# Optimization experiments

Hardware: AMD Instinct MI355X
Metric: run time of the kernel (lower is better)

Reference implementation:

```python
import jax, jax.numpy as jnp
import numpy as np

D = 1024      # d_model
H = 16        # n_heads
HD = D // H   # head_dim = 64
B = 2
NQ = 2048     # prod(spatial_shape_q)
NK = 2048     # prod(spatial_shape_kv)
SCALE_BASE_Q = 2 * NQ   # spatial_shape_q[0] * 2
SCALE_BASE_K = 2 * NK   # spatial_shape_kv[0] * 2
THETA = 10000.0         # theta_rescale_factor=1.0 -> theta unchanged


def _init_freqs(dim):
    # learned_freq=True: parameter initialized to standard rotary frequencies
    return 1.0 / (THETA ** (jnp.arange(0, dim, 2, dtype=jnp.float32) / dim))


def _rotate_half(x):
    # interleaved pair rotation: (x1, x2) -> (-x2, x1)
    x1 = x[..., ::2]
    x2 = x[..., 1::2]
    return jnp.stack((-x2, x1), axis=-1).reshape(x.shape)


def _apply_rope_xpos(x, freqs_param, scale_base, sign):
    # x: (B, H, N, HD); freqs_param: (HD//2,)
    n = x.shape[2]
    dim = x.shape[-1]
    t = jnp.arange(n, dtype=jnp.float32)
    freqs = jnp.repeat(t[:, None] * freqs_param[None, :], 2, axis=-1)  # (N, HD)
    # xpos length-extrapolatable scaling
    power = (t - n // 2) / scale_base                                   # (N,)
    sv = (jnp.arange(0, dim, 2, dtype=jnp.float32) + 0.4 * dim) / (1.4 * dim)
    scale = jnp.repeat(sv[None, :] ** power[:, None], 2, axis=-1) ** sign  # (N, HD)
    return x * jnp.cos(freqs) * scale + _rotate_half(x) * jnp.sin(freqs) * scale


def setup_inputs() -> dict:
    key = jax.random.key(0)
    ks = jax.random.split(key, 10)
    s = 0.02
    return {
        "q_seq": jax.random.normal(ks[0], (B, NQ, D), jnp.float32),
        "kv_seq": jax.random.normal(ks[1], (B, NK, D), jnp.float32),
        "Wq": jax.random.normal(ks[2], (D, D), jnp.float32) * s,
        "bq": jnp.zeros((D,), jnp.float32),
        "Wk": jax.random.normal(ks[3], (D, D), jnp.float32) * s,
        "bk": jnp.zeros((D,), jnp.float32),
        "Wv": jax.random.normal(ks[4], (D, D), jnp.float32) * s,
        "bv": jnp.zeros((D,), jnp.float32),
        "Wo": jax.random.normal(ks[5], (D, D), jnp.float32) * s,
        "bo": jnp.zeros((D,), jnp.float32),
        "freqs_q": _init_freqs(HD),
        "freqs_kv": _init_freqs(HD),
    }


def reference(q_seq, kv_seq, Wq, bq, Wk, bk, Wv, bv, Wo, bo, freqs_q, freqs_kv):
    Bq, Nq, C = q_seq.shape
    Nk = kv_seq.shape[1]
    q = (q_seq @ Wq.T + bq).reshape(Bq, Nq, H, HD).transpose(0, 2, 1, 3)
    k = (kv_seq @ Wk.T + bk).reshape(Bq, Nk, H, HD).transpose(0, 2, 1, 3)
    v = (kv_seq @ Wv.T + bv).reshape(Bq, Nk, H, HD).transpose(0, 2, 1, 3)
    q = _apply_rope_xpos(q, freqs_q, SCALE_BASE_Q, sign=1.0)   # queries: scale^{+1}
    k = _apply_rope_xpos(k, freqs_kv, SCALE_BASE_K, sign=-1.0)  # keys: scale^{-1}
    attn = jax.nn.softmax(
        jnp.einsum("bhqd,bhkd->bhqk", q, k) * (HD ** -0.5), axis=-1
    )
    out = jnp.einsum("bhqk,bhkd->bhqd", attn, v)
    out = out.transpose(0, 2, 1, 3).reshape(Bq, Nq, C)
    return (out @ Wo.T + bo, attn)
```

## Files before the change

kernel.cpp:

```cpp
#include <hip/hip_runtime.h>

#define NQ 2048
#define NKK 2048
#define DD 1024
#define HH 16

typedef __attribute__((ext_vector_type(8))) short bf16x8;
typedef __attribute__((ext_vector_type(4))) float f32x4;

__device__ __forceinline__ short f2bf(float f){
    union { float f; unsigned u; } v; v.f = f;
    unsigned u = v.u + 0x7FFFu + ((v.u >> 16) & 1u);
    return (short)(u >> 16);
}
__device__ __forceinline__ float bf2f(unsigned short u){
    union { unsigned u; float f; } v; v.u = ((unsigned)u) << 16;
    return v.f;
}

__global__ __launch_bounds__(256) void cvt_bf16(const float* __restrict__ src,
                                                short* __restrict__ dst, int n){
    int i = (blockIdx.x * 256 + threadIdx.x) * 4;
    if (i < n){
        float4 v = *(const float4*)(src + i);
        union { short s[4]; uint2 u; } o;
        o.s[0] = f2bf(v.x); o.s[1] = f2bf(v.y);
        o.s[2] = f2bf(v.z); o.s[3] = f2bf(v.w);
        *(uint2*)(dst + i) = o.u;
    }
}

__global__ __launch_bounds__(256) void rope_kernel(const short* __restrict__ x,
                                                   short* __restrict__ y,
                                                   const float* __restrict__ fr,
                                                   int N, float scale_base,
                                                   float sign, float prescale){
    int p = blockIdx.x * 256 + threadIdx.x;
    int col2 = p & 511;
    int row  = p >> 9;
    int n    = row & (N - 1);
    int i    = col2 & 31;
    float t  = (float)n;
    float fv = t * fr[i];
    float c = cosf(fv), s = sinf(fv);
    float power = (t - (float)(N / 2)) / scale_base;
    float sv = ((float)(2 * i) + 0.4f * 64.f) / (1.4f * 64.f);
    float scale = exp2f(sign * power * log2f(sv)) * prescale;
    unsigned xv = *(const unsigned*)(x + 2 * (size_t)p);
    float x0 = bf2f((unsigned short)(xv & 0xFFFFu));
    float x1 = bf2f((unsigned short)(xv >> 16));
    float y0 = (x0 * c - x1 * s) * scale;
    float y1 = (x1 * c + x0 * s) * scale;
    unsigned o = (unsigned)(unsigned short)f2bf(y0) |
                 ((unsigned)(unsigned short)f2bf(y1) << 16);
    *(unsigned*)(y + 2 * (size_t)p) = o;
}

template<bool F32OUT>
__global__ __launch_bounds__(256) void gemm_bt(const short* __restrict__ A,
                                               const short* __restrict__ W,
                                               const float* __restrict__ bias,
                                               void* __restrict__ Cout,
                                               int M, int N, int K){
    __shared__ __align__(16) short lA[128 * 72];
    __shared__ __align__(16) short lB[128 * 72];
    int tid = threadIdx.x;
    int wave = tid >> 6, lane = tid & 63;
    int l16 = lane & 15, quad = lane >> 4;
    int wr = wave >> 1, wc = wave & 1;
    int row0 = blockIdx.y * 128, col0 = blockIdx.x * 128;

    f32x4 acc[4][4];
#pragma unroll
    for (int a = 0; a < 4; a++)
#pragma unroll
        for (int b = 0; b < 4; b++) acc[a][b] = (f32x4){0.f, 0.f, 0.f, 0.f};

    for (int k0 = 0; k0 < K; k0 += 64){
#pragma unroll
        for (int r = 0; r < 4; r++){
            int e = r * 2048 + tid * 8;
            int ar = e >> 6, ac = e & 63;
            *(uint4*)&lA[ar * 72 + ac] = *(const uint4*)(A + (size_t)(row0 + ar) * K + k0 + ac);
            *(uint4*)&lB[ar * 72 + ac] = *(const uint4*)(W + (size_t)(col0 + ar) * K + k0 + ac);
        }
        __syncthreads();
#pragma unroll
        for (int kk = 0; kk < 2; kk++){
            bf16x8 af[4], bfr[4];
#pragma unroll
            for (int t = 0; t < 4; t++){
                af[t]  = *(const bf16x8*)&lA[(wr * 64 + t * 16 + l16) * 72 + kk * 32 + quad * 8];
                bfr[t] = *(const bf16x8*)&lB[(wc * 64 + t * 16 + l16) * 72 + kk * 32 + quad * 8];
            }
#pragma unroll
            for (int tm = 0; tm < 4; tm++)
#pragma unroll
                for (int tn = 0; tn < 4; tn++)
                    acc[tm][tn] = __builtin_amdgcn_mfma_f32_16x16x32_bf16(af[tm], bfr[tn], acc[tm][tn], 0, 0, 0);
        }
        __syncthreads();
    }
#pragma unroll
    for (int tm = 0; tm < 4; tm++){
        int gr = row0 + wr * 64 + tm * 16 + quad * 4;
#pragma unroll
        for (int tn = 0; tn < 4; tn++){
            int gc = col0 + wc * 64 + tn * 16 + l16;
            float bv = bias[gc];
#pragma unroll
            for (int r = 0; r < 4; r++){
                float v = acc[tm][tn][r] + bv;
                if (F32OUT) ((float*)Cout)[(size_t)(gr + r) * N + gc] = v;
                else        ((short*)Cout)[(size_t)(gr + r) * N + gc] = f2bf(v);
            }
        }
    }
}

__global__ __launch_bounds__(256) void transpose_v(const short* __restrict__ vp,
                                                   short* __restrict__ vT){
    int kt = blockIdx.x;
    int bh = blockIdx.y;
    int b = bh >> 4, h = bh & 15;
    int tid = threadIdx.x;
    int hd = tid & 63;
#pragma unroll
    for (int it = 0; it < 16; it++){
        int kl = (tid >> 6) + it * 4;
        int k = kt * 64 + kl;
        short v = vp[((size_t)(b * NKK + k)) * DD + h * 64 + hd];
        vT[((size_t)(bh * 64 + hd)) * NKK + k] = v;
    }
}

__global__ __launch_bounds__(256) void attn_kernel(const short* __restrict__ qp,
                                                   const short* __restrict__ kp,
                                                   const short* __restrict__ vT,
                                                   float* __restrict__ attn,
                                                   short* __restrict__ op){
    __shared__ __align__(16) short lK[64 * 72];
    __shared__ __align__(16) short lV[64 * 72];
    __shared__ __align__(16) short lP[64 * 72];
    __shared__ float lMf[64], lLi[64];

    int qt = blockIdx.x;
    int bh = blockIdx.y;
    int b = bh >> 4, h = bh & 15;
    int tid = threadIdx.x, wave = tid >> 6, lane = tid & 63;
    int l16 = lane & 15, quad = lane >> 4;

    int q0 = qt * 64;
    int qrow = q0 + wave * 16 + l16;
    const short* qb = qp + ((size_t)(b * NQ + qrow)) * DD + h * 64;
    bf16x8 qf[2];
    qf[0] = *(const bf16x8*)(qb + quad * 8);
    qf[1] = *(const bf16x8*)(qb + 32 + quad * 8);

    const short* kb = kp + ((size_t)(b * NKK)) * DD + h * 64;
    const short* vb = vT + ((size_t)(bh * 64)) * NKK;

    float m = -1e30f, l = 0.f;
    for (int kt = 0; kt < 32; kt++){
#pragma unroll
        for (int rnd = 0; rnd < 2; rnd++){
            int e = rnd * 2048 + tid * 8;
            int kr = e >> 6, kc = e & 63;
            *(uint4*)&lK[kr * 72 + kc] = *(const uint4*)(kb + (size_t)(kt * 64 + kr) * DD + kc);
        }
        __syncthreads();
        f32x4 St[4];
#pragma unroll
        for (int t = 0; t < 4; t++){
            f32x4 a = (f32x4){0.f, 0.f, 0.f, 0.f};
#pragma unroll
            for (int kk = 0; kk < 2; kk++){
                bf16x8 kf = *(const bf16x8*)&lK[(t * 16 + l16) * 72 + kk * 32 + quad * 8];
                a = __builtin_amdgcn_mfma_f32_16x16x32_bf16(kf, qf[kk], a, 0, 0, 0);
            }
            St[t] = a;
        }
        float mx = m;
#pragma unroll
        for (int t = 0; t < 4; t++)
#pragma unroll
            for (int r = 0; r < 4; r++) mx = fmaxf(mx, St[t][r]);
        float sum = 0.f;
#pragma unroll
        for (int t = 0; t < 4; t++)
#pragma unroll
            for (int r = 0; r < 4; r++) sum += __expf(St[t][r] - mx);
        l = l * __expf(m - mx) + sum;
        m = mx;
        __syncthreads();
    }
    float M = fmaxf(m, __shfl_xor(m, 16, 64));
    M = fmaxf(M, __shfl_xor(M, 32, 64));
    float ls = l * __expf(m - M);
    ls += __shfl_xor(ls, 16, 64);
    ls += __shfl_xor(ls, 32, 64);
    if (quad == 0){ lMf[wave * 16 + l16] = M; lLi[wave * 16 + l16] = 1.f / ls; }
    __syncthreads();
    float mf[4], il[4];
#pragma unroll
    for (int r = 0; r < 4; r++){
        mf[r] = lMf[wave * 16 + quad * 4 + r];
        il[r] = lLi[wave * 16 + quad * 4 + r];
    }

    f32x4 O[4];
#pragma unroll
    for (int th = 0; th < 4; th++) O[th] = (f32x4){0.f, 0.f, 0.f, 0.f};
    float* ab = attn + (((size_t)bh * NQ) + q0 + wave * 16) * NKK;

    for (int kt = 0; kt < 32; kt++){
#pragma unroll
        for (int rnd = 0; rnd < 2; rnd++){
            int e = rnd * 2048 + tid * 8;
            int kr = e >> 6, kc = e & 63;
            *(uint4*)&lK[kr * 72 + kc] = *(const uint4*)(kb + (size_t)(kt * 64 + kr) * DD + kc);
            *(uint4*)&lV[kr * 72 + kc] = *(const uint4*)(vb + (size_t)kr * NKK + kt * 64 + kc);
        }
        __syncthreads();
        f32x4 S[4];
#pragma unroll
        for (int tn = 0; tn < 4; tn++){
            f32x4 a = (f32x4){0.f, 0.f, 0.f, 0.f};
#pragma unroll
            for (int kk = 0; kk < 2; kk++){
                bf16x8 kf = *(const bf16x8*)&lK[(tn * 16 + l16) * 72 + kk * 32 + quad * 8];
                a = __builtin_amdgcn_mfma_f32_16x16x32_bf16(qf[kk], kf, a, 0, 0, 0);
            }
            S[tn] = a;
        }
#pragma unroll
        for (int tn = 0; tn < 4; tn++){
#pragma unroll
            for (int r = 0; r < 4; r++){
                float p = __expf(S[tn][r] - mf[r]) * il[r];
                ab[(size_t)(quad * 4 + r) * NKK + kt * 64 + tn * 16 + l16] = p;
                lP[(wave * 16 + quad * 4 + r) * 72 + tn * 16 + l16] = f2bf(p);
            }
        }
#pragma unroll
        for (int kk = 0; kk < 2; kk++){
            bf16x8 pf = *(const bf16x8*)&lP[(wave * 16 + l16) * 72 + kk * 32 + quad * 8];
#pragma unroll
            for (int th = 0; th < 4; th++){
                bf16x8 vf = *(const bf16x8*)&lV[(th * 16 + l16) * 72 + kk * 32 + quad * 8];
                O[th] = __builtin_amdgcn_mfma_f32_16x16x32_bf16(pf, vf, O[th], 0, 0, 0);
            }
        }
        __syncthreads();
    }
#pragma unroll
    for (int th = 0; th < 4; th++){
#pragma unroll
        for (int r = 0; r < 4; r++){
            int q = q0 + wave * 16 + quad * 4 + r;
            op[((size_t)(b * NQ + q)) * DD + h * 64 + th * 16 + l16] = f2bf(O[th][r]);
        }
    }
}

extern "C" void kernel_launch(void* const* d_in, const int* in_sizes, int n_in,
                              void* d_out, int out_size, void* d_ws, size_t ws_size,
                              hipStream_t stream) {
    const float* q_seq = (const float*)d_in[0];
    const float* kv_seq = (const float*)d_in[1];
    const float* Wq = (const float*)d_in[2];
    const float* bq = (const float*)d_in[3];
    const float* Wk = (const float*)d_in[4];
    const float* bk = (const float*)d_in[5];
    const float* Wv = (const float*)d_in[6];
    const float* bv = (const float*)d_in[7];
    const float* Wo = (const float*)d_in[8];
    const float* bo = (const float*)d_in[9];
    const float* freqs_q = (const float*)d_in[10];
    const float* freqs_kv = (const float*)d_in[11];

    float* out0 = (float*)d_out;
    float* attn = (float*)d_out + 4194304;

    short* qb  = (short*)d_ws;
    short* kvb = qb  + 4194304;
    short* wqb = kvb + 4194304;
    short* wkb = wqb + 1048576;
    short* wvb = wkb + 1048576;
    short* wob = wvb + 1048576;
    short* tmp = wob + 1048576;
    short* qpb = tmp + 4194304;
    short* kpb = qpb + 4194304;
    short* vpb = kpb + 4194304;
    short* vTb = qb;
    short* opb = tmp;

    cvt_bf16<<<4096, 256, 0, stream>>>(q_seq, qb, 4194304);
    cvt_bf16<<<4096, 256, 0, stream>>>(kv_seq, kvb, 4194304);
    cvt_bf16<<<1024, 256, 0, stream>>>(Wq, wqb, 1048576);
    cvt_bf16<<<1024, 256, 0, stream>>>(Wk, wkb, 1048576);
    cvt_bf16<<<1024, 256, 0, stream>>>(Wv, wvb, 1048576);
    cvt_bf16<<<1024, 256, 0, stream>>>(Wo, wob, 1048576);

    dim3 ggrid(8, 32);
    gemm_bt<false><<<ggrid, 256, 0, stream>>>(qb, wqb, bq, tmp, 4096, 1024, 1024);
    rope_kernel<<<8192, 256, 0, stream>>>(tmp, qpb, freqs_q, NQ, 4096.f, 1.f, 0.125f);
    gemm_bt<false><<<ggrid, 256, 0, stream>>>(kvb, wkb, bk, tmp, 4096, 1024, 1024);
    rope_kernel<<<8192, 256, 0, stream>>>(tmp, kpb, freqs_kv, NKK, 4096.f, -1.f, 1.f);
    gemm_bt<false><<<ggrid, 256, 0, stream>>>(kvb, wvb, bv, vpb, 4096, 1024, 1024);
    transpose_v<<<dim3(32, 32), 256, 0, stream>>>(vpb, vTb);
    attn_kernel<<<dim3(32, 32), 256, 0, stream>>>(qpb, kpb, vTb, attn, opb);
    gemm_bt<true><<<ggrid, 256, 0, stream>>>(opb, wob, bo, out0, 4096, 1024, 1024);
}
```

Measured before the change: 887.8 us.

## Use direct global-to-LDS loads, double-buffer GEMM, tile V transpose, vectorize attn stores

The GEMM switches to global_load_lds direct loads into double-buffered unpadded LDS tiles, so the next K tile is prefetched while the current one is computed. The V transpose now goes through an LDS tile, giving coalesced 16-byte reads and writes. The attention kernel loads K/V with direct-to-LDS loads and stages the fp32 probabilities in LDS, so the attn matrix is written with vectorized nontemporal 16-byte stores instead of scattered scalar stores. Removing the LDS padding may add bank conflicts on fragment reads, and the larger fp32 staging buffer raises LDS use.

```diff
diff --git a/kernel.cpp b/kernel.cpp
--- a/kernel.cpp
+++ b/kernel.cpp
@@ -16,6 +16,13 @@
 __device__ __forceinline__ float bf2f(unsigned short u){
     union { unsigned u; float f; } v; v.u = ((unsigned)u) << 16;
     return v.f;
+}
+
+__device__ __forceinline__ void gload16(const void* g, void* l){
+    __builtin_amdgcn_global_load_lds(
+        (__attribute__((address_space(1))) void*)g,
+        (__attribute__((address_space(3))) void*)l,
+        16, 0, 0);
 }
 
 __global__ __launch_bounds__(256) void cvt_bf16(const float* __restrict__ src,
@@ -62,36 +69,48 @@
                                                const float* __restrict__ bias,
                                                void* __restrict__ Cout,
                                                int M, int N, int K){
-    __shared__ __align__(16) short lA[128 * 72];
-    __shared__ __align__(16) short lB[128 * 72];
+    __shared__ __align__(16) short lA[2][128 * 64];
+    __shared__ __align__(16) short lB[2][128 * 64];
     int tid = threadIdx.x;
     int wave = tid >> 6, lane = tid & 63;
     int l16 = lane & 15, quad = lane >> 4;
     int wr = wave >> 1, wc = wave & 1;
     int row0 = blockIdx.y * 128, col0 = blockIdx.x * 128;
 
+    const short* Ab = A + (size_t)(row0 + wave * 32 + (lane >> 3)) * K + (lane & 7) * 8;
+    const short* Wb = W + (size_t)(col0 + wave * 32 + (lane >> 3)) * K + (lane & 7) * 8;
+
     f32x4 acc[4][4];
 #pragma unroll
     for (int a = 0; a < 4; a++)
 #pragma unroll
         for (int b = 0; b < 4; b++) acc[a][b] = (f32x4){0.f, 0.f, 0.f, 0.f};
 
-    for (int k0 = 0; k0 < K; k0 += 64){
-#pragma unroll
-        for (int r = 0; r < 4; r++){
-            int e = r * 2048 + tid * 8;
-            int ar = e >> 6, ac = e & 63;
-            *(uint4*)&lA[ar * 72 + ac] = *(const uint4*)(A + (size_t)(row0 + ar) * K + k0 + ac);
-            *(uint4*)&lB[ar * 72 + ac] = *(const uint4*)(W + (size_t)(col0 + ar) * K + k0 + ac);
-        }
-        __syncthreads();
+    int nt = K >> 6;
+#pragma unroll
+    for (int i = 0; i < 4; i++){
+        gload16(Ab + (size_t)i * 8 * K, &lA[0][(wave * 32 + i * 8) * 64]);
+        gload16(Wb + (size_t)i * 8 * K, &lB[0][(wave * 32 + i * 8) * 64]);
+    }
+    __syncthreads();
+
+    for (int t = 0; t < nt; t++){
+        int cur = t & 1;
+        if (t + 1 < nt){
+            int k0 = (t + 1) << 6;
+#pragma unroll
+            for (int i = 0; i < 4; i++){
+                gload16(Ab + (size_t)i * 8 * K + k0, &lA[cur ^ 1][(wave * 32 + i * 8) * 64]);
+                gload16(Wb + (size_t)i * 8 * K + k0, &lB[cur ^ 1][(wave * 32 + i * 8) * 64]);
+            }
+        }
 #pragma unroll
         for (int kk = 0; kk < 2; kk++){
             bf16x8 af[4], bfr[4];
 #pragma unroll
-            for (int t = 0; t < 4; t++){
-                af[t]  = *(const bf16x8*)&lA[(wr * 64 + t * 16 + l16) * 72 + kk * 32 + quad * 8];
-                bfr[t] = *(const bf16x8*)&lB[(wc * 64 + t * 16 + l16) * 72 + kk * 32 + quad * 8];
+            for (int t4 = 0; t4 < 4; t4++){
+                af[t4]  = *(const bf16x8*)&lA[cur][(wr * 64 + t4 * 16 + l16) * 64 + kk * 32 + quad * 8];
+                bfr[t4] = *(const bf16x8*)&lB[cur][(wc * 64 + t4 * 16 + l16) * 64 + kk * 32 + quad * 8];
             }
 #pragma unroll
             for (int tm = 0; tm < 4; tm++)
@@ -101,6 +120,7 @@
         }
         __syncthreads();
     }
+
 #pragma unroll
     for (int tm = 0; tm < 4; tm++){
         int gr = row0 + wr * 64 + tm * 16 + quad * 4;
@@ -120,28 +140,37 @@
 
 __global__ __launch_bounds__(256) void transpose_v(const short* __restrict__ vp,
                                                    short* __restrict__ vT){
+    __shared__ __align__(16) short tl[64 * 66];
     int kt = blockIdx.x;
     int bh = blockIdx.y;
     int b = bh >> 4, h = bh & 15;
     int tid = threadIdx.x;
-    int hd = tid & 63;
-#pragma unroll
-    for (int it = 0; it < 16; it++){
-        int kl = (tid >> 6) + it * 4;
-        int k = kt * 64 + kl;
-        short v = vp[((size_t)(b * NKK + k)) * DD + h * 64 + hd];
-        vT[((size_t)(bh * 64 + hd)) * NKK + k] = v;
-    }
-}
-
-__global__ __launch_bounds__(256) void attn_kernel(const short* __restrict__ qp,
-                                                   const short* __restrict__ kp,
-                                                   const short* __restrict__ vT,
-                                                   float* __restrict__ attn,
-                                                   short* __restrict__ op){
-    __shared__ __align__(16) short lK[64 * 72];
-    __shared__ __align__(16) short lV[64 * 72];
-    __shared__ __align__(16) short lP[64 * 72];
+    const short* src = vp + ((size_t)(b * NKK + kt * 64)) * DD + h * 64;
+#pragma unroll
+    for (int rd = 0; rd < 2; rd++){
+        int kl = (tid >> 3) + rd * 32, c8 = (tid & 7) * 8;
+        *(uint4*)&tl[kl * 66 + c8] = *(const uint4*)(src + (size_t)kl * DD + c8);
+    }
+    __syncthreads();
+    short* dst = vT + ((size_t)(bh * 64)) * NKK + kt * 64;
+#pragma unroll
+    for (int rd = 0; rd < 2; rd++){
+        int hd = (tid >> 3) + rd * 32, k8 = (tid & 7) * 8;
+        union { short s[8]; uint4 u; } o;
+#pragma unroll
+        for (int j = 0; j < 8; j++) o.s[j] = tl[(k8 + j) * 66 + hd];
+        *(uint4*)(dst + (size_t)hd * NKK + k8) = o.u;
+    }
+}
+
+__global__ __launch_bounds__(256, 4) void attn_kernel(const short* __restrict__ qp,
+                                                      const short* __restrict__ kp,
+                                                      const short* __restrict__ vT,
+                                                      float* __restrict__ attn,
+                                                      short* __restrict__ op){
+    __shared__ __align__(16) short lK[64 * 64];
+    __shared__ __align__(16) short lV[64 * 64];
+    __shared__ __align__(16) float lPf[64 * 68];
     __shared__ float lMf[64], lLi[64];
 
     int qt = blockIdx.x;
@@ -163,11 +192,9 @@
     float m = -1e30f, l = 0.f;
     for (int kt = 0; kt < 32; kt++){
 #pragma unroll
-        for (int rnd = 0; rnd < 2; rnd++){
-            int e = rnd * 2048 + tid * 8;
-            int kr = e >> 6, kc = e & 63;
-            *(uint4*)&lK[kr * 72 + kc] = *(const uint4*)(kb + (size_t)(kt * 64 + kr) * DD + kc);
-        }
+        for (int i = 0; i < 2; i++)
+            gload16(kb + (size_t)(kt * 64 + wave * 16 + i * 8 + (lane >> 3)) * DD + (lane & 7) * 8,
+                    &lK[(wave * 16 + i * 8) * 64]);
         __syncthreads();
         f32x4 St[4];
 #pragma unroll
@@ -175,7 +202,7 @@
             f32x4 a = (f32x4){0.f, 0.f, 0.f, 0.f};
 #pragma unroll
             for (int kk = 0; kk < 2; kk++){
-                bf16x8 kf = *(const bf16x8*)&lK[(t * 16 + l16) * 72 + kk * 32 + quad * 8];
+                bf16x8 kf = *(const bf16x8*)&lK[(t * 16 + l16) * 64 + kk * 32 + quad * 8];
                 a = __builtin_amdgcn_mfma_f32_16x16x32_bf16(kf, qf[kk], a, 0, 0, 0);
             }
             St[t] = a;
@@ -215,11 +242,11 @@
 
     for (int kt = 0; kt < 32; kt++){
 #pragma unroll
-        for (int rnd = 0; rnd < 2; rnd++){
-            int e = rnd * 2048 + tid * 8;
-            int kr = e >> 6, kc = e & 63;
-            *(uint4*)&lK[kr * 72 + kc] = *(const uint4*)(kb + (size_t)(kt * 64 + kr) * DD + kc);
-            *(uint4*)&lV[kr * 72 + kc] = *(const uint4*)(vb + (size_t)kr * NKK + kt * 64 + kc);
+        for (int i = 0; i < 2; i++){
+            gload16(kb + (size_t)(kt * 64 + wave * 16 + i * 8 + (lane >> 3)) * DD + (lane & 7) * 8,
+                    &lK[(wave * 16 + i * 8) * 64]);
+            gload16(vb + (size_t)(wave * 16 + i * 8 + (lane >> 3)) * NKK + kt * 64 + (lane & 7) * 8,
+                    &lV[(wave * 16 + i * 8) * 64]);
         }
         __syncthreads();
         f32x4 S[4];
@@ -228,27 +255,34 @@
             f32x4 a = (f32x4){0.f, 0.f, 0.f, 0.f};
 #pragma unroll
             for (int kk = 0; kk < 2; kk++){
-                bf16x8 kf = *(const bf16x8*)&lK[(tn * 16 + l16) * 72 + kk * 32 + quad * 8];
+                bf16x8 kf = *(const bf16x8*)&lK[(tn * 16 + l16) * 64 + kk * 32 + quad * 8];
                 a = __builtin_amdgcn_mfma_f32_16x16x32_bf16(qf[kk], kf, a, 0, 0, 0);
             }
             S[tn] = a;
         }
 #pragma unroll
-        for (int tn = 0; tn < 4; tn++){
-#pragma unroll
-            for (int r = 0; r < 4; r++){
-                float p = __expf(S[tn][r] - mf[r]) * il[r];
-                ab[(size_t)(quad * 4 + r) * NKK + kt * 64 + tn * 16 + l16] = p;
-                lP[(wave * 16 + quad * 4 + r) * 72 + tn * 16 + l16] = f2bf(p);
-            }
+        for (int tn = 0; tn < 4; tn++)
+#pragma unroll
+            for (int r = 0; r < 4; r++)
+                lPf[(wave * 16 + quad * 4 + r) * 68 + tn * 16 + l16] =
+                    __expf(S[tn][r] - mf[r]) * il[r];
+#pragma unroll
+        for (int j = 0; j < 4; j++){
+            f32x4 pv = *(const f32x4*)&lPf[(wave * 16 + j * 4 + quad) * 68 + l16 * 4];
+            __builtin_nontemporal_store(pv,
+                (f32x4*)&ab[(size_t)(j * 4 + quad) * NKK + kt * 64 + l16 * 4]);
         }
 #pragma unroll
         for (int kk = 0; kk < 2; kk++){
-            bf16x8 pf = *(const bf16x8*)&lP[(wave * 16 + l16) * 72 + kk * 32 + quad * 8];
+            f32x4 p0 = *(const f32x4*)&lPf[(wave * 16 + l16) * 68 + kk * 32 + quad * 8];
+            f32x4 p1 = *(const f32x4*)&lPf[(wave * 16 + l16) * 68 + kk * 32 + quad * 8 + 4];
+            union { short s[8]; bf16x8 v; } pf;
+#pragma unroll
+            for (int r = 0; r < 4; r++){ pf.s[r] = f2bf(p0[r]); pf.s[4 + r] = f2bf(p1[r]); }
 #pragma unroll
             for (int th = 0; th < 4; th++){
-                bf16x8 vf = *(const bf16x8*)&lV[(th * 16 + l16) * 72 + kk * 32 + quad * 8];
-                O[th] = __builtin_amdgcn_mfma_f32_16x16x32_bf16(pf, vf, O[th], 0, 0, 0);
+                bf16x8 vf = *(const bf16x8*)&lV[(th * 16 + l16) * 64 + kk * 32 + quad * 8];
+                O[th] = __builtin_amdgcn_mfma_f32_16x16x32_bf16(pf.v, vf, O[th], 0, 0, 0);
             }
         }
         __syncthreads();
```

After: 754.4 us. 15.0% less time.
